# Optimization experiments

Measured on AMD Instinct MI355X. Metric: run time of the kernel, lower is better.

## Reference

```python
import jax, jax.numpy as jnp
import numpy as np

B, T, D = 2, 2048, 1024
H, HD = 16, 32
INNER = H * HD
FF = 4 * D
KT, KP = 3, 15


def _layernorm(x, g, b, eps=1e-5):
    mu = jnp.mean(x, axis=-1, keepdims=True)
    var = jnp.var(x, axis=-1, keepdims=True)
    return (x - mu) * jax.lax.rsqrt(var + eps) * g + b


def _causal_dwconv(x, w, b):
    # x: (b,t,d), w: (d,1,k) depthwise kernel; causal left-pad of k-1
    k = w.shape[-1]
    xc = jnp.transpose(x, (0, 2, 1))  # (b,d,t)
    xp = jnp.pad(xc, ((0, 0), (0, 0), (k - 1, 0)))
    y = jax.lax.conv_general_dilated(
        xp, w, window_strides=(1,), padding='VALID',
        feature_group_count=x.shape[-1],
        dimension_numbers=('NCH', 'OIH', 'NCH'))
    return jnp.transpose(y + b[None, :, None], (0, 2, 1))


def _causal_linear_attention(q, k, v, mask):
    # q,k,v: (b,t,h,d); mask: (b,t)
    m = mask[:, :, None, None]
    q = (jax.nn.elu(q) + 1.0) * m
    k = (jax.nn.elu(k) + 1.0) * m
    v = v * m
    kv = jnp.einsum('bthd,bthe->bthde', k, v)
    kv_prefix = jnp.cumsum(kv, axis=1)          # (b,t,h,d,e) large intermediate
    k_prefix = jnp.cumsum(k, axis=1)
    num = jnp.einsum('bthd,bthde->bthe', q, kv_prefix)
    den = jnp.sum(q * k_prefix, axis=-1, keepdims=True)
    return (num / (den + 1e-6)) * m


def setup_inputs() -> dict:
    key = jax.random.key(0)
    ks = jax.random.split(key, 10)
    w = lambda i, shape: jax.random.normal(ks[i], shape, jnp.float32) * 0.02
    return {
        'inputs': jax.random.normal(ks[0], (B, T, D), jnp.float32),
        'mask': jnp.ones((B, T), jnp.float32),
        'ln1_g': jnp.ones((D,), jnp.float32), 'ln1_b': jnp.zeros((D,), jnp.float32),
        'W_in': w(1, (D, D + 3 * INNER)), 'b_in': jnp.zeros((D + 3 * INNER,), jnp.float32),
        'W_c': w(2, (INNER, D)), 'b_c': jnp.zeros((D,), jnp.float32),
        'w_t': w(3, (D, 1, KT)), 'b_t': jnp.zeros((D,), jnp.float32),
        'w_p': w(4, (D, 1, KP)), 'b_p': jnp.zeros((D,), jnp.float32),
        'W_mix': w(5, (3 * D, D)), 'b_mix': jnp.zeros((D,), jnp.float32),
        'ln2_g': jnp.ones((D,), jnp.float32), 'ln2_b': jnp.zeros((D,), jnp.float32),
        'W1': w(6, (D, FF)), 'b1': jnp.zeros((FF,), jnp.float32),
        'W2': w(7, (FF, D)), 'b2': jnp.zeros((D,), jnp.float32),
    }


def reference(inputs, mask, ln1_g, ln1_b, W_in, b_in, W_c, b_c, w_t, b_t,
              w_p, b_p, W_mix, b_mix, ln2_g, ln2_b, W1, b1, W2, b2):
    residual = inputs
    normed = _layernorm(inputs, ln1_g, ln1_b)
    proj = normed @ W_in + b_in
    gate, q, k, v = jnp.split(proj, [D, D + INNER, D + 2 * INNER], axis=-1)
    b, t, _ = inputs.shape
    q = q.reshape(b, t, H, HD)
    k = k.reshape(b, t, H, HD)
    v = v.reshape(b, t, H, HD)
    content = _causal_linear_attention(q, k, v, mask).reshape(b, t, INNER)
    content = content @ W_c + b_c
    temporal = _causal_dwconv(normed, w_t, b_t)
    positional = _causal_dwconv(normed, w_p, b_p)
    mixed = jnp.concatenate((content, temporal, positional), axis=-1) @ W_mix + b_mix
    mask_f = mask[:, :, None]
    out = residual + jax.nn.sigmoid(gate) * mixed  # dropout=0.0 -> identity
    out = out * mask_f
    h = _layernorm(out, ln2_g, ln2_b)
    ffn = jax.nn.gelu(h @ W1 + b1, approximate=False) @ W2 + b2
    out = out + ffn
    return out * mask_f
```

## Files before the change

### kernel.cpp

```cpp
#include <hip/hip_runtime.h>
#include <math.h>

#define BB 2
#define TT 2048
#define DD 1024
#define HH 16
#define INNERD 512
#define FFD 4096
#define NPROJ 2560
#define CATD 3072
#define MROWS (BB*TT)
#define CHUNK 64
#define NCH (TT/CHUNK)
#define BH 32

typedef __bf16 bf16;
typedef __attribute__((ext_vector_type(8))) __bf16 bf16x8;
typedef __attribute__((ext_vector_type(4))) __bf16 bf16x4;
typedef __attribute__((ext_vector_type(4))) float f32x4;

struct Part4 { void* p0; void* p1; void* p2; void* p3; };

__global__ __launch_bounds__(256) void prep_fused(
    const float* __restrict__ inputs, const float* __restrict__ ln1_g,
    const float* __restrict__ ln1_b, bf16* __restrict__ normed,
    const float* __restrict__ W_in,  bf16* __restrict__ wt_in,
    const float* __restrict__ W_c,   bf16* __restrict__ wt_c,
    const float* __restrict__ W_mix, bf16* __restrict__ wt_mix,
    const float* __restrict__ W1,    bf16* __restrict__ wt1,
    const float* __restrict__ W2,    bf16* __restrict__ wt2)
{
    int blk = blockIdx.x, tid = threadIdx.x;
    if (blk < MROWS) {
        int row = blk;
        f32x4 xv = ((const f32x4*)(inputs + (size_t)row * DD))[tid];
        float s = xv[0] + xv[1] + xv[2] + xv[3];
        float s2 = xv[0]*xv[0] + xv[1]*xv[1] + xv[2]*xv[2] + xv[3]*xv[3];
        #pragma unroll
        for (int off = 32; off > 0; off >>= 1) {
            s  += __shfl_xor(s,  off, 64);
            s2 += __shfl_xor(s2, off, 64);
        }
        __shared__ float rs[4], rs2[4];
        int wid = tid >> 6;
        if ((tid & 63) == 0) { rs[wid] = s; rs2[wid] = s2; }
        __syncthreads();
        s  = rs[0] + rs[1] + rs[2] + rs[3];
        s2 = rs2[0] + rs2[1] + rs2[2] + rs2[3];
        float mean = s * (1.0f / DD);
        float var  = s2 * (1.0f / DD) - mean * mean;
        float rstd = rsqrtf(var + 1e-5f);
        f32x4 gv = ((const f32x4*)ln1_g)[tid];
        f32x4 bv = ((const f32x4*)ln1_b)[tid];
        bf16x4 o;
        #pragma unroll
        for (int q = 0; q < 4; q++)
            o[q] = (bf16)((xv[q] - mean) * rstd * gv[q] + bv[q]);
        ((bf16x4*)(normed + (size_t)row * DD))[tid] = o;
        return;
    }
    int tb = blk - MROWS;
    const float* W; bf16* Wt; int Kd, Nd;
    if      (tb < 2560)  {             W = W_in;  Wt = wt_in;  Kd = 1024; Nd = 2560; }
    else if (tb < 3072)  { tb -= 2560; W = W_c;   Wt = wt_c;   Kd = 512;  Nd = 1024; }
    else if (tb < 6144)  { tb -= 3072; W = W_mix; Wt = wt_mix; Kd = 3072; Nd = 1024; }
    else if (tb < 10240) { tb -= 6144; W = W1;    Wt = wt1;    Kd = 1024; Nd = 4096; }
    else                 { tb -= 10240;W = W2;    Wt = wt2;    Kd = 4096; Nd = 1024; }
    int ntx = Nd >> 5;
    int nb = (tb % ntx) * 32, kb = (tb / ntx) * 32;
    __shared__ float t[32][33];
    int tx = tid & 31, ty = tid >> 5;
    #pragma unroll
    for (int r = 0; r < 32; r += 8)
        t[ty + r][tx] = W[(size_t)(kb + ty + r) * Nd + nb + tx];
    __syncthreads();
    #pragma unroll
    for (int r = 0; r < 32; r += 8)
        Wt[(size_t)(nb + ty + r) * Kd + kb + tx] = (bf16)t[tx][ty + r];
}

__device__ __forceinline__ void stage_half(
    const bf16* __restrict__ src, int ld, int k0, int h_row0,
    bf16* lds_half, int wave, int rl, int ce)
{
    #pragma unroll
    for (int i = 0; i < 2; i++) {
        int R = h_row0 + (i * 8 + wave) * 8 + rl;
        const bf16* g = src + (size_t)R * ld + k0 + ce;
        __builtin_amdgcn_global_load_lds(
            (const __attribute__((address_space(1))) void*)g,
            (__attribute__((address_space(3))) void*)(lds_half + (i * 8 + wave) * 512),
            16, 0, 0);
    }
}

__device__ __forceinline__ bf16x8 frag_ld(const bf16* buf, int row, int col)
{
    int off = row * 64 + col;
    off ^= ((row >> 2) & 1) << 4;
    return *(const bf16x8*)(buf + off);
}

template<int EPI>
__global__ __launch_bounds__(512) void gemm256(
    const bf16* __restrict__ A,  int lda,
    const bf16* __restrict__ Bt, int ldb,
    const float* __restrict__ bias,
    bf16* __restrict__ Cb, int ldc,
    int K, Part4 part)
{
    __shared__ bf16 sA0[16384], sB0[16384], sA1[16384], sB1[16384];
    const int tid  = threadIdx.x;
    const int wave = tid >> 6, lane = tid & 63;
    const int m0 = blockIdx.x * 256, n0 = blockIdx.y * 256;
    A  += (size_t)m0 * lda + (size_t)blockIdx.z * K;
    Bt += (size_t)n0 * ldb + (size_t)blockIdx.z * K;
    const int wr = wave >> 2, wc = wave & 3;
    const int rl = lane >> 3;
    const int ce = ((lane & 7) * 8) ^ ((lane >= 32) ? 16 : 0);
    const int fm = lane & 15;
    const int fk = (lane >> 4) * 8;

    f32x4 acc[8][4];
    #pragma unroll
    for (int i = 0; i < 8; i++)
        #pragma unroll
        for (int j = 0; j < 4; j++)
            acc[i][j] = (f32x4){0.f, 0.f, 0.f, 0.f};

    const int NT = K >> 6;
    stage_half(A,  lda, 0, 0,   sA0,        wave, rl, ce);
    stage_half(A,  lda, 0, 128, sA0 + 8192, wave, rl, ce);
    stage_half(Bt, ldb, 0, 0,   sB0,        wave, rl, ce);
    stage_half(Bt, ldb, 0, 128, sB0 + 8192, wave, rl, ce);
    if (NT > 1) {
        stage_half(A, lda, 64, 0, sA1, wave, rl, ce);
        asm volatile("s_waitcnt vmcnt(2)" ::: "memory");
    } else {
        asm volatile("s_waitcnt vmcnt(0)" ::: "memory");
    }
    __builtin_amdgcn_s_barrier();

    for (int t = 0; t < NT; t++) {
        bf16* Ac = (t & 1) ? sA1 : sA0;
        bf16* Bc = (t & 1) ? sB1 : sB0;
        bf16* An = (t & 1) ? sA0 : sA1;
        bf16* Bn = (t & 1) ? sB0 : sB1;
        const int kn = (t + 1) << 6;
        bf16x8 bq[4][2];
        #pragma unroll
        for (int p = 0; p < 4; p++) {
            bf16x8 aq[2][2];
            if (p == 0) {
                #pragma unroll
                for (int j = 0; j < 4; j++)
                    #pragma unroll
                    for (int ks = 0; ks < 2; ks++)
                        bq[j][ks] = frag_ld(Bc, wc * 64 + j * 16 + fm, ks * 32 + fk);
            }
            #pragma unroll
            for (int ii = 0; ii < 2; ii++)
                #pragma unroll
                for (int ks = 0; ks < 2; ks++)
                    aq[ii][ks] = frag_ld(Ac, wr * 128 + (p * 2 + ii) * 16 + fm,
                                         ks * 32 + fk);
            if (t + 1 < NT) {
                if (p == 0) stage_half(A,  lda, kn, 128, An + 8192, wave, rl, ce);
                if (p == 1) stage_half(Bt, ldb, kn, 0,   Bn,        wave, rl, ce);
                if (p == 2) stage_half(Bt, ldb, kn, 128, Bn + 8192, wave, rl, ce);
            }
            __builtin_amdgcn_s_barrier();
            asm volatile("s_waitcnt lgkmcnt(0)" ::: "memory");
            __builtin_amdgcn_sched_barrier(0);
            __builtin_amdgcn_s_setprio(1);
            #pragma unroll
            for (int ii = 0; ii < 2; ii++)
                #pragma unroll
                for (int j = 0; j < 4; j++)
                    #pragma unroll
                    for (int ks = 0; ks < 2; ks++)
                        acc[p * 2 + ii][j] = __builtin_amdgcn_mfma_f32_16x16x32_bf16(
                            aq[ii][ks], bq[j][ks], acc[p * 2 + ii][j], 0, 0, 0);
            __builtin_amdgcn_s_setprio(0);
            __builtin_amdgcn_s_barrier();
        }
        if (t + 2 < NT)
            stage_half(A, lda, (t + 2) << 6, 0, Ac, wave, rl, ce);
        if (t + 1 < NT) {
            if (t + 2 < NT) asm volatile("s_waitcnt vmcnt(2)" ::: "memory");
            else            asm volatile("s_waitcnt vmcnt(0)" ::: "memory");
            __builtin_amdgcn_s_barrier();
        }
    }

    void* psel = nullptr;
    if constexpr (EPI == 4) {
        int z = blockIdx.z;
        psel = (z == 0) ? part.p0 : (z == 1) ? part.p1 : (z == 2) ? part.p2 : part.p3;
    }

    #pragma unroll
    for (int i = 0; i < 8; i++) {
        int mbase = m0 + wr * 128 + i * 16 + (lane >> 4) * 4;
        #pragma unroll
        for (int j = 0; j < 4; j++) {
            int col = n0 + wc * 64 + j * 16 + fm;
            float bv = 0.f;
            if constexpr (EPI == 0 || EPI == 1) bv = bias[col];
            #pragma unroll
            for (int r = 0; r < 4; r++) {
                int row = mbase + r;
                float v = acc[i][j][r] + bv;
                if constexpr (EPI == 0) {
                    Cb[(size_t)row * ldc + col] = (bf16)v;
                } else if constexpr (EPI == 1) {
                    float z2 = v * (1.5957691f + 0.07135502f * v * v);
                    v = v / (1.0f + __expf(-z2));
                    Cb[(size_t)row * ldc + col] = (bf16)v;
                } else {
                    ((bf16*)psel)[(size_t)row * DD + col] = (bf16)v;
                }
            }
        }
    }
}

__global__ __launch_bounds__(256) void epi_wc(
    const bf16* __restrict__ P0, const bf16* __restrict__ P1,
    const float* __restrict__ bias, bf16* __restrict__ cat)
{
    int id = blockIdx.x * 256 + threadIdx.x;
    int row = id >> 8, cg = id & 255;
    bf16x4 s0 = ((const bf16x4*)P0)[id];
    bf16x4 s1 = ((const bf16x4*)P1)[id];
    f32x4 b  = ((const f32x4*)bias)[cg];
    bf16x4 o;
    #pragma unroll
    for (int q = 0; q < 4; q++) o[q] = (bf16)((float)s0[q] + (float)s1[q] + b[q]);
    *(bf16x4*)(cat + (size_t)row * CATD + cg * 4) = o;
}

__global__ __launch_bounds__(256) void epi_mix_ln2(
    const bf16* __restrict__ P0, const bf16* __restrict__ P1,
    const bf16* __restrict__ P2, const float* __restrict__ bias,
    const bf16* __restrict__ proj, const float* __restrict__ res,
    const float* __restrict__ mask,
    const float* __restrict__ g2, const float* __restrict__ b2v,
    float* __restrict__ out1, bf16* __restrict__ hbuf)
{
    int row = blockIdx.x, tid = threadIdx.x;
    float m = mask[row];
    size_t off = (size_t)row * DD + tid * 4;
    bf16x4 s0 = *(const bf16x4*)(P0 + off);
    bf16x4 s1 = *(const bf16x4*)(P1 + off);
    bf16x4 s2v = *(const bf16x4*)(P2 + off);
    f32x4 bv = ((const f32x4*)bias)[tid];
    bf16x4 g4 = *(const bf16x4*)(proj + (size_t)row * NPROJ + tid * 4);
    f32x4 rv = ((const f32x4*)(res + (size_t)row * DD))[tid];
    f32x4 v;
    #pragma unroll
    for (int q = 0; q < 4; q++) {
        float sg = 1.0f / (1.0f + __expf(-(float)g4[q]));
        float sv = (float)s0[q] + (float)s1[q] + (float)s2v[q] + bv[q];
        v[q] = (rv[q] + sg * sv) * m;
    }
    ((f32x4*)(out1 + (size_t)row * DD))[tid] = v;
    float s = v[0] + v[1] + v[2] + v[3];
    float s2 = v[0]*v[0] + v[1]*v[1] + v[2]*v[2] + v[3]*v[3];
    #pragma unroll
    for (int off2 = 32; off2 > 0; off2 >>= 1) {
        s  += __shfl_xor(s,  off2, 64);
        s2 += __shfl_xor(s2, off2, 64);
    }
    __shared__ float rs[4], rs2[4];
    int wid = tid >> 6;
    if ((tid & 63) == 0) { rs[wid] = s; rs2[wid] = s2; }
    __syncthreads();
    s  = rs[0] + rs[1] + rs[2] + rs[3];
    s2 = rs2[0] + rs2[1] + rs2[2] + rs2[3];
    float mean = s * (1.0f / DD);
    float var  = s2 * (1.0f / DD) - mean * mean;
    float rstd = rsqrtf(var + 1e-5f);
    f32x4 gg = ((const f32x4*)g2)[tid];
    f32x4 bb = ((const f32x4*)b2v)[tid];
    bf16x4 h;
    #pragma unroll
    for (int q = 0; q < 4; q++)
        h[q] = (bf16)((v[q] - mean) * rstd * gg[q] + bb[q]);
    ((bf16x4*)(hbuf + (size_t)row * DD))[tid] = h;
}

__global__ __launch_bounds__(256) void epi_w2(
    float* __restrict__ d_out, const float* __restrict__ out1,
    const bf16* __restrict__ P0, const bf16* __restrict__ P1,
    const bf16* __restrict__ P2, const bf16* __restrict__ P3,
    const float* __restrict__ bias, const float* __restrict__ mask)
{
    int id = blockIdx.x * 256 + threadIdx.x;
    int row = id >> 8;
    float m = mask[row];
    bf16x4 a0 = ((const bf16x4*)P0)[id];
    bf16x4 a1 = ((const bf16x4*)P1)[id];
    bf16x4 a2 = ((const bf16x4*)P2)[id];
    bf16x4 a3 = ((const bf16x4*)P3)[id];
    f32x4 r = ((const f32x4*)out1)[id];
    f32x4 b = ((const f32x4*)bias)[id & 255];
    f32x4 o;
    #pragma unroll
    for (int q = 0; q < 4; q++) {
        float sv = (float)a0[q] + (float)a1[q] + (float)a2[q] + (float)a3[q];
        o[q] = (r[q] + sv + b[q]) * m;
    }
    ((f32x4*)d_out)[id] = o;
}

__device__ __forceinline__ float phi_f(float x) {
    return x > 0.f ? x + 1.f : __expf(x);
}

__global__ __launch_bounds__(256) void mid_fused(
    const bf16* __restrict__ x,
    const float* __restrict__ w_t, const float* __restrict__ b_t,
    const float* __restrict__ w_p, const float* __restrict__ b_p,
    bf16* __restrict__ cat,
    const bf16* __restrict__ proj, const float* __restrict__ mask,
    float* __restrict__ kvsum, float* __restrict__ kssum)
{
    __shared__ float s_ks[2][CHUNK][32], s_vs[2][CHUNK][32];
    int blk = blockIdx.x, tid = threadIdx.x;
    if (blk < 1024) {
        int id = blk * 256 + tid;
        int cg = id & 127, rp = id >> 7;
        int c0 = cg * 8;
        int row0 = rp * 2;
        int t0 = row0 & (TT - 1);
        bf16x8 xw[16];
        #pragma unroll
        for (int j = 0; j < 16; j++) {
            int t = t0 - 14 + j;
            if (t >= 0)
                xw[j] = *(const bf16x8*)(x + (size_t)(row0 - 14 + j) * DD + c0);
            else
                #pragma unroll
                for (int q = 0; q < 8; q++) xw[j][q] = (bf16)0.f;
        }
        float y15[2][8], y3[2][8];
        #pragma unroll
        for (int q = 0; q < 8; q++) {
            float bp = b_p[c0 + q], bt = b_t[c0 + q];
            y15[0][q] = bp; y15[1][q] = bp;
            y3[0][q] = bt;  y3[1][q] = bt;
        }
        #pragma unroll
        for (int i = 0; i < 15; i++) {
            float wp[8];
            #pragma unroll
            for (int q = 0; q < 8; q++) wp[q] = w_p[(c0 + q) * 15 + i];
            #pragma unroll
            for (int rr = 0; rr < 2; rr++)
                #pragma unroll
                for (int q = 0; q < 8; q++)
                    y15[rr][q] = fmaf(wp[q], (float)xw[rr + i][q], y15[rr][q]);
        }
        #pragma unroll
        for (int i = 0; i < 3; i++) {
            float wt[8];
            #pragma unroll
            for (int q = 0; q < 8; q++) wt[q] = w_t[(c0 + q) * 3 + i];
            #pragma unroll
            for (int rr = 0; rr < 2; rr++)
                #pragma unroll
                for (int q = 0; q < 8; q++)
                    y3[rr][q] = fmaf(wt[q], (float)xw[rr + 12 + i][q], y3[rr][q]);
        }
        #pragma unroll
        for (int rr = 0; rr < 2; rr++) {
            bf16x8 o3, o15;
            #pragma unroll
            for (int q = 0; q < 8; q++) { o3[q] = (bf16)y3[rr][q]; o15[q] = (bf16)y15[rr][q]; }
            *(bf16x8*)(cat + (size_t)(row0 + rr) * CATD + DD + c0)     = o3;
            *(bf16x8*)(cat + (size_t)(row0 + rr) * CATD + 2 * DD + c0) = o15;
        }
        return;
    }
    int w = tid >> 6;
    if (w >= 2) return;
    int lane = tid & 63;
    int ci = (blk - 1024) * 2 + w;
    int c  = ci & (NCH - 1);
    int bh = ci >> 5;
    int b  = bh >> 4, hh = bh & (HH - 1);
    float (*ks)[32] = s_ks[w];
    float (*vs)[32] = s_vs[w];
    int row0 = b * TT + c * CHUNK;
    {
        int row = row0 + lane;
        float m = mask[row];
        const bf16* kp = proj + (size_t)row * NPROJ + DD + INNERD + hh * 32;
        const bf16* vp = kp + INNERD;
        #pragma unroll
        for (int s = 0; s < 4; s++) {
            bf16x8 k8 = *(const bf16x8*)(kp + s * 8);
            bf16x8 v8 = *(const bf16x8*)(vp + s * 8);
            #pragma unroll
            for (int q = 0; q < 8; q++) {
                ks[lane][s * 8 + q] = phi_f((float)k8[q]) * m;
                vs[lane][s * 8 + q] = (float)v8[q] * m;
            }
        }
    }
    int e = lane & 31, d0 = (lane >> 5) * 16;
    float kv[16], ksl[16];
    #pragma unroll
    for (int j = 0; j < 16; j++) { kv[j] = 0.f; ksl[j] = 0.f; }
    for (int t = 0; t < CHUNK; t++) {
        float ve = vs[t][e];
        f32x4 kr[4];
        #pragma unroll
        for (int s = 0; s < 4; s++) kr[s] = *(const f32x4*)&ks[t][d0 + s * 4];
        #pragma unroll
        for (int j = 0; j < 16; j++) {
            float kval = kr[j >> 2][j & 3];
            kv[j] = fmaf(kval, ve, kv[j]);
            ksl[j] += kval;
        }
    }
    size_t base = (size_t)ci * 1024;
    #pragma unroll
    for (int j = 0; j < 16; j++)
        kvsum[base + (size_t)(d0 + j) * 32 + e] = kv[j];
    if (e == 0) {
        #pragma unroll
        for (int j = 0; j < 16; j++)
            kssum[ci * 32 + d0 + j] = ksl[j];
    }
}

__global__ __launch_bounds__(256) void attn_prefix(
    const float* __restrict__ kvsum, const float* __restrict__ kssum,
    float* __restrict__ kvpref, float* __restrict__ kspref)
{
    int bh = blockIdx.x;
    int tid = threadIdx.x;
    float run[4] = {0.f, 0.f, 0.f, 0.f};
    for (int c = 0; c < NCH; c++) {
        size_t base = (size_t)(bh * NCH + c) * 1024 + tid * 4;
        #pragma unroll
        for (int q = 0; q < 4; q++) {
            kvpref[base + q] = run[q];
            run[q] += kvsum[base + q];
        }
    }
    if (tid < 32) {
        float r = 0.f;
        for (int c = 0; c < NCH; c++) {
            kspref[(bh * NCH + c) * 32 + tid] = r;
            r += kssum[(bh * NCH + c) * 32 + tid];
        }
    }
}

__global__ __launch_bounds__(64) void attn_scan(
    const bf16* __restrict__ proj, const float* __restrict__ mask,
    const float* __restrict__ kvpref, const float* __restrict__ kspref,
    bf16* __restrict__ attn_out)
{
    int blk = blockIdx.x;
    int c  = blk & (NCH - 1);
    int bh = blk >> 5;
    int b  = bh >> 4, hh = bh & (HH - 1);
    int lane = threadIdx.x;
    __shared__ float qs[CHUNK][32], ks[CHUNK][32], vs[CHUNK][32];
    __shared__ float ms[CHUNK];
    int row0 = b * TT + c * CHUNK;
    {
        int row = row0 + lane;
        float m = mask[row];
        ms[lane] = m;
        const bf16* qp = proj + (size_t)row * NPROJ + DD + hh * 32;
        const bf16* kp = qp + INNERD;
        const bf16* vp = kp + INNERD;
        #pragma unroll
        for (int s = 0; s < 4; s++) {
            bf16x8 q8 = *(const bf16x8*)(qp + s * 8);
            bf16x8 k8 = *(const bf16x8*)(kp + s * 8);
            bf16x8 v8 = *(const bf16x8*)(vp + s * 8);
            #pragma unroll
            for (int q = 0; q < 8; q++) {
                qs[lane][s * 8 + q] = phi_f((float)q8[q]) * m;
                ks[lane][s * 8 + q] = phi_f((float)k8[q]) * m;
                vs[lane][s * 8 + q] = (float)v8[q] * m;
            }
        }
    }
    int e = lane & 31, d0 = (lane >> 5) * 16;
    float kv[16], ksl[16];
    size_t base = (size_t)blk * 1024;
    #pragma unroll
    for (int j = 0; j < 16; j++) kv[j] = kvpref[base + (size_t)(d0 + j) * 32 + e];
    #pragma unroll
    for (int j = 0; j < 16; j++) ksl[j] = kspref[blk * 32 + d0 + j];
    __syncthreads();
    for (int t = 0; t < CHUNK; t++) {
        float ve = vs[t][e];
        f32x4 kr[4], qr[4];
        #pragma unroll
        for (int s = 0; s < 4; s++) kr[s] = *(const f32x4*)&ks[t][d0 + s * 4];
        #pragma unroll
        for (int s = 0; s < 4; s++) qr[s] = *(const f32x4*)&qs[t][d0 + s * 4];
        float num0 = 0.f, num1 = 0.f, den0 = 0.f, den1 = 0.f;
        #pragma unroll
        for (int j = 0; j < 16; j++) {
            float kval = kr[j >> 2][j & 3], qval = qr[j >> 2][j & 3];
            kv[j]  = fmaf(kval, ve, kv[j]);
            ksl[j] += kval;
            if (j & 1) { num1 = fmaf(qval, kv[j], num1); den1 = fmaf(qval, ksl[j], den1); }
            else       { num0 = fmaf(qval, kv[j], num0); den0 = fmaf(qval, ksl[j], den0); }
        }
        float num = num0 + num1, den = den0 + den1;
        num += __shfl_xor(num, 32, 64);
        den += __shfl_xor(den, 32, 64);
        if (lane < 32)
            attn_out[(size_t)(row0 + t) * INNERD + hh * 32 + e] =
                (bf16)(num / (den + 1e-6f) * ms[t]);
    }
}

extern "C" void kernel_launch(void* const* d_in, const int* in_sizes, int n_in,
                              void* d_out, int out_size, void* d_ws, size_t ws_size,
                              hipStream_t stream)
{
    const float* inputs = (const float*)d_in[0];
    const float* mask   = (const float*)d_in[1];
    const float* ln1_g  = (const float*)d_in[2];
    const float* ln1_b  = (const float*)d_in[3];
    const float* W_in   = (const float*)d_in[4];
    const float* b_in   = (const float*)d_in[5];
    const float* W_c    = (const float*)d_in[6];
    const float* b_c    = (const float*)d_in[7];
    const float* w_t    = (const float*)d_in[8];
    const float* b_t    = (const float*)d_in[9];
    const float* w_p    = (const float*)d_in[10];
    const float* b_p    = (const float*)d_in[11];
    const float* W_mix  = (const float*)d_in[12];
    const float* b_mix  = (const float*)d_in[13];
    const float* ln2_g  = (const float*)d_in[14];
    const float* ln2_b  = (const float*)d_in[15];
    const float* W1     = (const float*)d_in[16];
    const float* b1     = (const float*)d_in[17];
    const float* W2     = (const float*)d_in[18];
    const float* b2     = (const float*)d_in[19];
    float* out = (float*)d_out;

    char* p = (char*)d_ws;
    bf16* normed = (bf16*)p;  p += (size_t)MROWS * DD * 2;
    bf16* proj   = (bf16*)p;  p += (size_t)MROWS * NPROJ * 2;
    bf16* attnb  = (bf16*)p;  p += (size_t)MROWS * INNERD * 2;
    bf16* cat    = (bf16*)p;  p += (size_t)MROWS * CATD * 2;
    float* out1  = (float*)p; p += (size_t)MROWS * DD * 4;
    bf16* hbuf   = (bf16*)p;  p += (size_t)MROWS * DD * 2;
    bf16* wt_in  = (bf16*)p;  p += (size_t)NPROJ * DD * 2;
    bf16* wt_c   = (bf16*)p;  p += (size_t)DD * INNERD * 2;
    bf16* wt_mix = (bf16*)p;  p += (size_t)DD * CATD * 2;
    bf16* wt1    = (bf16*)p;  p += (size_t)FFD * DD * 2;
    bf16* wt2    = (bf16*)p;  p += (size_t)DD * FFD * 2;
    bf16* ffn1   = (bf16*)d_ws;
    float* kvsum = out1;
    float* kvpref= kvsum  + (size_t)BH * NCH * 1024;
    float* kssum = kvpref + (size_t)BH * NCH * 1024;
    float* kspref= kssum  + (size_t)BH * NCH * 32;
    bf16*  c_p0  = (bf16*)d_out;
    bf16*  c_p1  = (bf16*)out1;
    bf16*  m_p0  = (bf16*)d_out;
    bf16*  m_p1  = (bf16*)d_out + (size_t)MROWS * DD;
    bf16*  m_p2  = hbuf;
    bf16*  w2_p0 = cat;
    bf16*  w2_p1 = cat + (size_t)MROWS * DD;
    bf16*  w2_p2 = cat + (size_t)MROWS * DD * 2;
    bf16*  w2_p3 = hbuf;

    prep_fused<<<MROWS + 14336, 256, 0, stream>>>(
        inputs, ln1_g, ln1_b, normed,
        W_in, wt_in, W_c, wt_c, W_mix, wt_mix, W1, wt1, W2, wt2);
    gemm256<0><<<dim3(MROWS/256, NPROJ/256), 512, 0, stream>>>(
        normed, DD, wt_in, DD, b_in, proj, NPROJ, DD, Part4{});
    mid_fused<<<1024 + 512, 256, 0, stream>>>(
        normed, w_t, b_t, w_p, b_p, cat, proj, mask, kvsum, kssum);
    attn_prefix<<<BH, 256, 0, stream>>>(kvsum, kssum, kvpref, kspref);
    attn_scan  <<<BH * NCH, 64, 0, stream>>>(proj, mask, kvpref, kspref, attnb);
    gemm256<4><<<dim3(MROWS/256, DD/256, 2), 512, 0, stream>>>(
        attnb, INNERD, wt_c, INNERD, nullptr, nullptr, DD, INNERD / 2,
        Part4{c_p0, c_p1, nullptr, nullptr});
    epi_wc<<<MROWS * DD / 4 / 256, 256, 0, stream>>>(c_p0, c_p1, b_c, cat);
    gemm256<4><<<dim3(MROWS/256, DD/256, 3), 512, 0, stream>>>(
        cat, CATD, wt_mix, CATD, nullptr, nullptr, DD, CATD / 3,
        Part4{m_p0, m_p1, m_p2, nullptr});
    epi_mix_ln2<<<MROWS, 256, 0, stream>>>(m_p0, m_p1, m_p2, b_mix, proj, inputs,
                                           mask, ln2_g, ln2_b, out1, hbuf);
    gemm256<1><<<dim3(MROWS/256, FFD/256), 512, 0, stream>>>(
        hbuf, DD, wt1, DD, b1, ffn1, FFD, DD, Part4{});
    gemm256<4><<<dim3(MROWS/256, DD/256, 4), 512, 0, stream>>>(
        ffn1, FFD, wt2, FFD, nullptr, nullptr, DD, FFD / 4,
        Part4{w2_p0, w2_p1, w2_p2, w2_p3});
    epi_w2<<<MROWS * DD / 4 / 256, 256, 0, stream>>>(out, out1, w2_p0, w2_p1,
                                                     w2_p2, w2_p3, b2, mask);
}
```

Before: 434.2 us.

## Switch GEMM to K=32 tiles with four-stage LDS ring buffer

The 256x256 GEMM mainloop moves from double-buffered K=64 tiles to a four-slot ring of K=32 tiles, prefetching three tiles ahead, with a new XOR swizzle for the LDS layout and fragment loads. The aim is deeper global-to-LDS prefetch, so memory latency is better hidden behind MFMA work. The cost is more barriers per unit of K work and fewer MFMAs between synchronisation points. The loop is unrolled by four and assumes K/32 is a multiple of four.

After: 414.7 us. 4.5% less time.

```diff
diff --git a/kernel.cpp b/kernel.cpp
--- a/kernel.cpp
+++ b/kernel.cpp
@@ -79,26 +79,76 @@
         Wt[(size_t)(nb + ty + r) * Kd + kb + tx] = (bf16)t[tx][ty + r];
 }
 
-__device__ __forceinline__ void stage_half(
-    const bf16* __restrict__ src, int ld, int k0, int h_row0,
-    bf16* lds_half, int wave, int rl, int ce)
+__device__ __forceinline__ void stage_tile32(
+    const bf16* __restrict__ src, int ld, int k0,
+    bf16* lds, int wave, int lane)
 {
     #pragma unroll
     for (int i = 0; i < 2; i++) {
-        int R = h_row0 + (i * 8 + wave) * 8 + rl;
-        const bf16* g = src + (size_t)R * ld + k0 + ce;
+        int rp = (i * 8 + wave) * 8 + (lane >> 3);
+        int x  = (lane & 7) ^ (rp & 7);
+        int r  = rp * 2 + ((x >> 2) & 1);
+        int cc = x & 3;
+        const bf16* g = src + (size_t)r * ld + k0 + cc * 8;
         __builtin_amdgcn_global_load_lds(
             (const __attribute__((address_space(1))) void*)g,
-            (__attribute__((address_space(3))) void*)(lds_half + (i * 8 + wave) * 512),
+            (__attribute__((address_space(3))) void*)(lds + (i * 8 + wave) * 512),
             16, 0, 0);
     }
 }
 
-__device__ __forceinline__ bf16x8 frag_ld(const bf16* buf, int row, int col)
-{
-    int off = row * 64 + col;
-    off ^= ((row >> 2) & 1) << 4;
-    return *(const bf16x8*)(buf + off);
+__device__ __forceinline__ bf16x8 frag32(const bf16* buf, int row, int cc)
+{
+    int off16 = (row >> 1) * 8 + ((((row & 1) << 2) | cc) ^ ((row >> 1) & 7));
+    return *(const bf16x8*)(buf + off16 * 8);
+}
+
+__device__ __forceinline__ void tile_step(
+    int t, int NT, const bf16* __restrict__ A, int lda,
+    const bf16* __restrict__ Bt, int ldb,
+    const bf16* Acur, const bf16* Bcur, bf16* Ast, bf16* Bst,
+    int wave, int lane, int wr, int wc, f32x4 (&acc)[8][4])
+{
+    const int fm = lane & 15, cc = lane >> 4;
+    bf16x8 bq[4], aq[4];
+    #pragma unroll
+    for (int j = 0; j < 4; j++) bq[j] = frag32(Bcur, wc * 64 + j * 16 + fm, cc);
+    #pragma unroll
+    for (int i = 0; i < 4; i++) aq[i] = frag32(Acur, wr * 128 + i * 16 + fm, cc);
+    if (t + 3 < NT) stage_tile32(A, lda, (t + 3) * 32, Ast, wave, lane);
+    __builtin_amdgcn_s_barrier();
+    asm volatile("s_waitcnt lgkmcnt(0)" ::: "memory");
+    __builtin_amdgcn_sched_barrier(0);
+    __builtin_amdgcn_s_setprio(1);
+    #pragma unroll
+    for (int i = 0; i < 4; i++)
+        #pragma unroll
+        for (int j = 0; j < 4; j++)
+            acc[i][j] = __builtin_amdgcn_mfma_f32_16x16x32_bf16(
+                aq[i], bq[j], acc[i][j], 0, 0, 0);
+    __builtin_amdgcn_s_setprio(0);
+    __builtin_amdgcn_s_barrier();
+    #pragma unroll
+    for (int i = 0; i < 4; i++) aq[i] = frag32(Acur, wr * 128 + (4 + i) * 16 + fm, cc);
+    if (t + 3 < NT) stage_tile32(Bt, ldb, (t + 3) * 32, Bst, wave, lane);
+    __builtin_amdgcn_s_barrier();
+    asm volatile("s_waitcnt lgkmcnt(0)" ::: "memory");
+    __builtin_amdgcn_sched_barrier(0);
+    __builtin_amdgcn_s_setprio(1);
+    #pragma unroll
+    for (int i = 0; i < 4; i++)
+        #pragma unroll
+        for (int j = 0; j < 4; j++)
+            acc[4 + i][j] = __builtin_amdgcn_mfma_f32_16x16x32_bf16(
+                aq[i], bq[j], acc[4 + i][j], 0, 0, 0);
+    __builtin_amdgcn_s_setprio(0);
+    __builtin_amdgcn_s_barrier();
+    if (t + 1 < NT) {
+        if (t + 3 < NT)      asm volatile("s_waitcnt vmcnt(8)" ::: "memory");
+        else if (t + 2 < NT) asm volatile("s_waitcnt vmcnt(4)" ::: "memory");
+        else                 asm volatile("s_waitcnt vmcnt(0)" ::: "memory");
+        __builtin_amdgcn_s_barrier();
+    }
 }
 
 template<int EPI>
@@ -109,17 +159,14 @@
     bf16* __restrict__ Cb, int ldc,
     int K, Part4 part)
 {
-    __shared__ bf16 sA0[16384], sB0[16384], sA1[16384], sB1[16384];
+    __shared__ bf16 sA[4][8192], sB[4][8192];
     const int tid  = threadIdx.x;
     const int wave = tid >> 6, lane = tid & 63;
     const int m0 = blockIdx.x * 256, n0 = blockIdx.y * 256;
     A  += (size_t)m0 * lda + (size_t)blockIdx.z * K;
     Bt += (size_t)n0 * ldb + (size_t)blockIdx.z * K;
     const int wr = wave >> 2, wc = wave & 3;
-    const int rl = lane >> 3;
-    const int ce = ((lane & 7) * 8) ^ ((lane >= 32) ? 16 : 0);
     const int fm = lane & 15;
-    const int fk = (lane >> 4) * 8;
 
     f32x4 acc[8][4];
     #pragma unroll
@@ -128,69 +175,25 @@
         for (int j = 0; j < 4; j++)
             acc[i][j] = (f32x4){0.f, 0.f, 0.f, 0.f};
 
-    const int NT = K >> 6;
-    stage_half(A,  lda, 0, 0,   sA0,        wave, rl, ce);
-    stage_half(A,  lda, 0, 128, sA0 + 8192, wave, rl, ce);
-    stage_half(Bt, ldb, 0, 0,   sB0,        wave, rl, ce);
-    stage_half(Bt, ldb, 0, 128, sB0 + 8192, wave, rl, ce);
-    if (NT > 1) {
-        stage_half(A, lda, 64, 0, sA1, wave, rl, ce);
-        asm volatile("s_waitcnt vmcnt(2)" ::: "memory");
-    } else {
-        asm volatile("s_waitcnt vmcnt(0)" ::: "memory");
-    }
+    const int NT = K >> 5;
+    stage_tile32(A,  lda, 0,  sA[0], wave, lane);
+    stage_tile32(Bt, ldb, 0,  sB[0], wave, lane);
+    stage_tile32(A,  lda, 32, sA[1], wave, lane);
+    stage_tile32(Bt, ldb, 32, sB[1], wave, lane);
+    stage_tile32(A,  lda, 64, sA[2], wave, lane);
+    stage_tile32(Bt, ldb, 64, sB[2], wave, lane);
+    asm volatile("s_waitcnt vmcnt(8)" ::: "memory");
     __builtin_amdgcn_s_barrier();
 
-    for (int t = 0; t < NT; t++) {
-        bf16* Ac = (t & 1) ? sA1 : sA0;
-        bf16* Bc = (t & 1) ? sB1 : sB0;
-        bf16* An = (t & 1) ? sA0 : sA1;
-        bf16* Bn = (t & 1) ? sB0 : sB1;
-        const int kn = (t + 1) << 6;
-        bf16x8 bq[4][2];
-        #pragma unroll
-        for (int p = 0; p < 4; p++) {
-            bf16x8 aq[2][2];
-            if (p == 0) {
-                #pragma unroll
-                for (int j = 0; j < 4; j++)
-                    #pragma unroll
-                    for (int ks = 0; ks < 2; ks++)
-                        bq[j][ks] = frag_ld(Bc, wc * 64 + j * 16 + fm, ks * 32 + fk);
-            }
-            #pragma unroll
-            for (int ii = 0; ii < 2; ii++)
-                #pragma unroll
-                for (int ks = 0; ks < 2; ks++)
-                    aq[ii][ks] = frag_ld(Ac, wr * 128 + (p * 2 + ii) * 16 + fm,
-                                         ks * 32 + fk);
-            if (t + 1 < NT) {
-                if (p == 0) stage_half(A,  lda, kn, 128, An + 8192, wave, rl, ce);
-                if (p == 1) stage_half(Bt, ldb, kn, 0,   Bn,        wave, rl, ce);
-                if (p == 2) stage_half(Bt, ldb, kn, 128, Bn + 8192, wave, rl, ce);
-            }
-            __builtin_amdgcn_s_barrier();
-            asm volatile("s_waitcnt lgkmcnt(0)" ::: "memory");
-            __builtin_amdgcn_sched_barrier(0);
-            __builtin_amdgcn_s_setprio(1);
-            #pragma unroll
-            for (int ii = 0; ii < 2; ii++)
-                #pragma unroll
-                for (int j = 0; j < 4; j++)
-                    #pragma unroll
-                    for (int ks = 0; ks < 2; ks++)
-                        acc[p * 2 + ii][j] = __builtin_amdgcn_mfma_f32_16x16x32_bf16(
-                            aq[ii][ks], bq[j][ks], acc[p * 2 + ii][j], 0, 0, 0);
-            __builtin_amdgcn_s_setprio(0);
-            __builtin_amdgcn_s_barrier();
-        }
-        if (t + 2 < NT)
-            stage_half(A, lda, (t + 2) << 6, 0, Ac, wave, rl, ce);
-        if (t + 1 < NT) {
-            if (t + 2 < NT) asm volatile("s_waitcnt vmcnt(2)" ::: "memory");
-            else            asm volatile("s_waitcnt vmcnt(0)" ::: "memory");
-            __builtin_amdgcn_s_barrier();
-        }
+    for (int t = 0; t < NT; t += 4) {
+        tile_step(t + 0, NT, A, lda, Bt, ldb, sA[0], sB[0], sA[3], sB[3],
+                  wave, lane, wr, wc, acc);
+        tile_step(t + 1, NT, A, lda, Bt, ldb, sA[1], sB[1], sA[0], sB[0],
+                  wave, lane, wr, wc, acc);
+        tile_step(t + 2, NT, A, lda, Bt, ldb, sA[2], sB[2], sA[1], sB[1],
+                  wave, lane, wr, wc, acc);
+        tile_step(t + 3, NT, A, lda, Bt, ldb, sA[3], sB[3], sA[2], sB[2],
+                  wave, lane, wr, wc, acc);
     }
 
     void* psel = nullptr;
```
